# Kernel tuning notes

Hardware: AMD Instinct MI355X
Metric: run time of the kernel (lower is better)

## Reference

```python
import jax, jax.numpy as jnp
import numpy as np

B, T, H, V = 4, 512, 2048, 32000
BETA = 0.1          # KL coefficient vs reference model
EPS_LOW = 0.2       # PPO clip lower
EPS_HIGH = 0.2      # PPO clip upper
TEMP = 1.0          # logit temperature


def _per_token_logps(h, w, ids):
    # h: [B,T,H], w: [V,H], ids: [B,T] -> log p(token_id) per position
    logits = jnp.einsum('bth,vh->btv', h, w) / TEMP          # [B,T,V]
    logps = jax.nn.log_softmax(logits.astype(jnp.float32), axis=-1)
    return jnp.take_along_axis(logps, ids[..., None], axis=-1)[..., 0]  # [B,T]


def setup_inputs() -> dict:
    key = jax.random.key(0)
    k = jax.random.split(key, 6)
    x = jax.random.normal(k[0], (B, T, H), jnp.float32)
    ref_input = jax.random.normal(k[1], (B, T, H), jnp.float32)
    lin_weight = jax.random.normal(k[2], (V, H), jnp.float32) * (H ** -0.5)
    ref_weight = jax.random.normal(k[3], (V, H), jnp.float32) * (H ** -0.5)
    selected_token_ids = jax.random.randint(k[4], (B, T), 0, V)
    attention_mask = jnp.ones((B, T), jnp.int32)
    advantages = jax.random.normal(k[5], (B,), jnp.float32)
    return {
        'x': x,
        'lin_weight': lin_weight,
        'ref_input': ref_input,
        'ref_weight': ref_weight,
        'advantages': advantages,
        'selected_token_ids': selected_token_ids,
        'attention_mask': attention_mask,
    }


def reference(x, lin_weight, ref_input, ref_weight, advantages,
              selected_token_ids, attention_mask):
    # policy per-token log-probs (fused linear + log-softmax + gather)
    logps = _per_token_logps(x, lin_weight, selected_token_ids)            # [B,T]
    # reference model path runs under no_grad in the original
    ref_logps = jax.lax.stop_gradient(
        _per_token_logps(ref_input, ref_weight, selected_token_ids))      # [B,T]
    # old_per_token_logps=None -> detached current logps (ratio==1 in fwd)
    old_logps = jax.lax.stop_gradient(logps)

    coef1 = jnp.exp(logps - old_logps)
    coef2 = jnp.clip(coef1, 1.0 - EPS_LOW, 1.0 + EPS_HIGH)
    adv = advantages[:, None]                                             # [B,1]
    per_token_loss = -jnp.minimum(coef1 * adv, coef2 * adv)

    # KL(ref || policy) surrogate: exp(d) - d - 1 with d = ref - cur
    d = ref_logps - logps
    kl = jnp.exp(d) - d - 1.0
    per_token_loss = per_token_loss + BETA * kl

    mask = attention_mask.astype(jnp.float32)
    # loss_type='bnpo': global masked token mean
    loss = jnp.sum(per_token_loss * mask) / jnp.maximum(jnp.sum(mask), 1.0)
    return loss
```

## Files before the change

### kernel.cpp

```cpp
#include <hip/hip_runtime.h>
#include <hip/hip_bf16.h>

#define B_ 4
#define T_ 512
#define H_ 2048
#define V_ 32000
#define M_ (B_ * T_)
#define BETA_ 0.1f

#define BM 128
#define BN 128
#define BK 32
#define NTILES (V_ / BN)
#define NP (NTILES * 2)
#define NPAD 512
#define GRID_LIN 4096

typedef __attribute__((ext_vector_type(8))) short short8;
typedef __attribute__((ext_vector_type(4))) float f32x4;

__device__ __forceinline__ void async_copy16(const void* g, void* l) {
  __builtin_amdgcn_global_load_lds(
      (const __attribute__((address_space(1))) void*)g,
      (__attribute__((address_space(3))) void*)l, 16, 0, 0);
}

__device__ __forceinline__ unsigned short f2bf(float f) {
  unsigned int u = __float_as_uint(f);
  u += 0x7fffu + ((u >> 16) & 1u);
  return (unsigned short)(u >> 16);
}

__global__ void cvt_bf16_kernel(const float* __restrict__ in,
                                unsigned short* __restrict__ out, int n4) {
  int i = blockIdx.x * blockDim.x + threadIdx.x;
  if (i < n4) {
    float4 v = ((const float4*)in)[i];
    ushort4 o;
    o.x = f2bf(v.x); o.y = f2bf(v.y); o.z = f2bf(v.z); o.w = f2bf(v.w);
    ((ushort4*)out)[i] = o;
  }
}

__global__ void sel_kernel(const float* __restrict__ x, const float* __restrict__ w,
                           const float* __restrict__ rx, const float* __restrict__ rw,
                           const int* __restrict__ ids, float* __restrict__ sel) {
  int gw = (blockIdx.x * 256 + threadIdx.x) >> 6;
  int l = threadIdx.x & 63;
  int md = gw >> 11;
  int m = gw & (M_ - 1);
  const float* xr = (md ? rx : x) + (size_t)m * H_;
  const float* wr = (md ? rw : w) + (size_t)ids[m] * H_;
  float s = 0.0f;
#pragma unroll
  for (int it = 0; it < H_ / 256; ++it) {
    int k = it * 256 + l * 4;
    float4 a = *(const float4*)(xr + k);
    float4 b = *(const float4*)(wr + k);
    s += a.x * b.x + a.y * b.y + a.z * b.z + a.w * b.w;
  }
#pragma unroll
  for (int off = 32; off; off >>= 1) s += __shfl_xor(s, off, 64);
  if (l == 0) sel[md * M_ + m] = s;
}

__global__ __launch_bounds__(256) void gemm_lse_kernel(
    const unsigned short* __restrict__ A,
    const unsigned short* __restrict__ Bw,
    float* __restrict__ pmax,
    float* __restrict__ psum) {
  const int linear = blockIdx.x;
  const int nt = (linear & 7) + 8 * (linear >> 7);
  if (nt >= NTILES) return;
  const int mb = (linear >> 3) & 15;

  __shared__ char smem[(BM + BN) * BK * 2];
  char* As = smem;
  char* Bs = smem + BM * BK * 2;

  const int tid = threadIdx.x;
  const int w = tid >> 6, l = tid & 63;
  const int quad = l >> 4, lr = l & 15;
  const int m0 = mb * BM, n0 = nt * BN;
  const int wm = (w >> 1) * 64, wn = (w & 1) * 64;

  const int s0 = tid, s1 = tid + 256;
  const unsigned short* gA0 = A + (size_t)(m0 + (s0 & 127)) * H_ + (s0 >> 7) * 8;
  const unsigned short* gA1 = A + (size_t)(m0 + (s1 & 127)) * H_ + (s1 >> 7) * 8;
  const unsigned short* gB0 = Bw + (size_t)(n0 + (s0 & 127)) * H_ + (s0 >> 7) * 8;
  const unsigned short* gB1 = Bw + (size_t)(n0 + (s1 & 127)) * H_ + (s1 >> 7) * 8;
  char* lA0 = As + s0 * 16; char* lA1 = As + s1 * 16;
  char* lB0 = Bs + s0 * 16; char* lB1 = Bs + s1 * 16;

  f32x4 acc[4][4] = {};

  const char* aRd[4]; const char* bRd[4];
#pragma unroll
  for (int i = 0; i < 4; ++i) {
    aRd[i] = As + (quad * 128 + wm + i * 16 + lr) * 16;
    bRd[i] = Bs + (quad * 128 + wn + i * 16 + lr) * 16;
  }

  for (int kt = 0; kt < H_ / BK; ++kt) {
    async_copy16(gA0, lA0); async_copy16(gA1, lA1);
    async_copy16(gB0, lB0); async_copy16(gB1, lB1);
    gA0 += BK; gA1 += BK; gB0 += BK; gB1 += BK;
    __syncthreads();
    short8 af[4], bf[4];
#pragma unroll
    for (int i = 0; i < 4; ++i) af[i] = *(const short8*)aRd[i];
#pragma unroll
    for (int j = 0; j < 4; ++j) bf[j] = *(const short8*)bRd[j];
#pragma unroll
    for (int i = 0; i < 4; ++i)
#pragma unroll
      for (int j = 0; j < 4; ++j)
        acc[i][j] = __builtin_amdgcn_mfma_f32_16x16x32_bf16(af[i], bf[j], acc[i][j], 0, 0, 0);
    __syncthreads();
  }

  const int p_idx = nt * 2 + (w & 1);
#pragma unroll
  for (int i = 0; i < 4; ++i) {
#pragma unroll
    for (int r = 0; r < 4; ++r) {
      float vmax = fmaxf(fmaxf(acc[i][0][r], acc[i][1][r]),
                         fmaxf(acc[i][2][r], acc[i][3][r]));
#pragma unroll
      for (int off = 8; off; off >>= 1) vmax = fmaxf(vmax, __shfl_xor(vmax, off, 64));
      float s = __expf(acc[i][0][r] - vmax) + __expf(acc[i][1][r] - vmax) +
                __expf(acc[i][2][r] - vmax) + __expf(acc[i][3][r] - vmax);
#pragma unroll
      for (int off = 8; off; off >>= 1) s += __shfl_xor(s, off, 64);
      if (lr == 0) {
        int mg = m0 + wm + i * 16 + quad * 4 + r;
        pmax[(size_t)mg * NPAD + p_idx] = vmax;
        psum[(size_t)mg * NPAD + p_idx] = s;
      }
    }
  }
}

__global__ void lse_merge_kernel(
    const float* __restrict__ pmaxP, const float* __restrict__ psumP,
    const float* __restrict__ pmaxR, const float* __restrict__ psumR,
    const float* __restrict__ sel, float* __restrict__ lp) {
  int gw = (blockIdx.x * 256 + threadIdx.x) >> 6;
  int l = threadIdx.x & 63;
  int md = gw >> 11, m = gw & (M_ - 1);
  const float* pm = (md ? pmaxR : pmaxP) + (size_t)m * NPAD;
  const float* ps = (md ? psumR : psumP) + (size_t)m * NPAD;
  float mx = -3.0e38f, s = 0.0f;
  for (int p = l; p < NP; p += 64) {
    float a = pm[p], b = ps[p];
    float nm = fmaxf(mx, a);
    s = s * __expf(mx - nm) + b * __expf(a - nm);
    mx = nm;
  }
#pragma unroll
  for (int off = 32; off; off >>= 1) {
    float omx = __shfl_xor(mx, off, 64);
    float os  = __shfl_xor(s, off, 64);
    float nm = fmaxf(mx, omx);
    s = s * __expf(mx - nm) + os * __expf(omx - nm);
    mx = nm;
  }
  if (l == 0) lp[md * M_ + m] = sel[md * M_ + m] - (mx + __logf(s));
}

__global__ void loss_kernel(const float* __restrict__ lp,
                            const float* __restrict__ adv,
                            const int* __restrict__ mask,
                            float* __restrict__ out) {
  __shared__ float sp[16], sm[16];
  int t = threadIdx.x;
  float pt = 0.0f, mk = 0.0f;
  for (int m = t; m < M_; m += 1024) {
    float d = lp[M_ + m] - lp[m];
    float kl = __expf(d) - d - 1.0f;
    float mkm = (float)mask[m];
    pt += (-adv[m >> 9] + BETA_ * kl) * mkm;
    mk += mkm;
  }
#pragma unroll
  for (int off = 32; off; off >>= 1) {
    pt += __shfl_xor(pt, off, 64);
    mk += __shfl_xor(mk, off, 64);
  }
  int wv = t >> 6, l = t & 63;
  if (l == 0) { sp[wv] = pt; sm[wv] = mk; }
  __syncthreads();
  if (t == 0) {
    float a = 0.0f, b = 0.0f;
#pragma unroll
    for (int i = 0; i < 16; ++i) { a += sp[i]; b += sm[i]; }
    out[0] = a / fmaxf(b, 1.0f);
  }
}

extern "C" void kernel_launch(void* const* d_in, const int* in_sizes, int n_in,
                              void* d_out, int out_size, void* d_ws, size_t ws_size,
                              hipStream_t stream) {
  const float* x    = (const float*)d_in[0];
  const float* lw   = (const float*)d_in[1];
  const float* rx   = (const float*)d_in[2];
  const float* rw   = (const float*)d_in[3];
  const float* adv  = (const float*)d_in[4];
  const int*   ids  = (const int*)d_in[5];
  const int*   mask = (const int*)d_in[6];
  float* out = (float*)d_out;

  char* ws = (char*)d_ws;
  unsigned short* Wb = (unsigned short*)ws;
  unsigned short* xb = (unsigned short*)(ws + (size_t)V_ * H_ * 2);
  char* p0 = ws + (size_t)V_ * H_ * 2 + (size_t)M_ * H_ * 2;
  const size_t PSZ = (size_t)M_ * NPAD * 4;
  float* pmaxP = (float*)(p0);
  float* psumP = (float*)(p0 + 1 * PSZ);
  float* pmaxR = (float*)(p0 + 2 * PSZ);
  float* psumR = (float*)(p0 + 3 * PSZ);
  float* sel   = (float*)(p0 + 4 * PSZ);
  float* lp    = (float*)(p0 + 4 * PSZ + 2 * M_ * 4);

  const int n4x = M_ * H_ / 4, n4w = V_ * H_ / 4;

  cvt_bf16_kernel<<<(n4x + 255) / 256, 256, 0, stream>>>(x, xb, n4x);
  cvt_bf16_kernel<<<(n4w + 255) / 256, 256, 0, stream>>>(lw, Wb, n4w);
  sel_kernel<<<(2 * M_) / 4, 256, 0, stream>>>(x, lw, rx, rw, ids, sel);
  gemm_lse_kernel<<<GRID_LIN, 256, 0, stream>>>(xb, Wb, pmaxP, psumP);
  cvt_bf16_kernel<<<(n4x + 255) / 256, 256, 0, stream>>>(rx, xb, n4x);
  cvt_bf16_kernel<<<(n4w + 255) / 256, 256, 0, stream>>>(rw, Wb, n4w);
  gemm_lse_kernel<<<GRID_LIN, 256, 0, stream>>>(xb, Wb, pmaxR, psumR);

  lse_merge_kernel<<<(2 * M_) / 4, 256, 0, stream>>>(pmaxP, psumP, pmaxR, psumR,
                                                     sel, lp);
  loss_kernel<<<1, 1024, 0, stream>>>(lp, adv, mask, out);
}
```

Baseline: 1.665 ms.

## Double-buffer GEMM LDS tiles with async prefetch and merge bf16 conversion launches

After: 1.679 ms. Within noise of the previous version (+0.9%).

```diff
diff --git a/kernel.cpp b/kernel.cpp
--- a/kernel.cpp
+++ b/kernel.cpp
@@ -31,15 +31,18 @@
   return (unsigned short)(u >> 16);
 }
 
-__global__ void cvt_bf16_kernel(const float* __restrict__ in,
-                                unsigned short* __restrict__ out, int n4) {
+__global__ void cvt2_bf16_kernel(const float* __restrict__ inA,
+                                 unsigned short* __restrict__ outA, int n4a,
+                                 const float* __restrict__ inB,
+                                 unsigned short* __restrict__ outB, int n4b) {
   int i = blockIdx.x * blockDim.x + threadIdx.x;
-  if (i < n4) {
-    float4 v = ((const float4*)in)[i];
-    ushort4 o;
-    o.x = f2bf(v.x); o.y = f2bf(v.y); o.z = f2bf(v.z); o.w = f2bf(v.w);
-    ((ushort4*)out)[i] = o;
-  }
+  const float* in; unsigned short* out;
+  if (i < n4a) { in = inA; out = outA; }
+  else { i -= n4a; if (i >= n4b) return; in = inB; out = outB; }
+  float4 v = ((const float4*)in)[i];
+  ushort4 o;
+  o.x = f2bf(v.x); o.y = f2bf(v.y); o.z = f2bf(v.z); o.w = f2bf(v.w);
+  ((ushort4*)out)[i] = o;
 }
 
 __global__ void sel_kernel(const float* __restrict__ x, const float* __restrict__ w,
@@ -74,9 +77,9 @@
   if (nt >= NTILES) return;
   const int mb = (linear >> 3) & 15;
 
-  __shared__ char smem[(BM + BN) * BK * 2];
-  char* As = smem;
-  char* Bs = smem + BM * BK * 2;
+  __shared__ char smem[32768];
+  char* As0 = smem;          char* As1 = smem + 8192;
+  char* Bs0 = smem + 16384;  char* Bs1 = smem + 24576;
 
   const int tid = threadIdx.x;
   const int w = tid >> 6, l = tid & 63;
@@ -85,39 +88,55 @@
   const int wm = (w >> 1) * 64, wn = (w & 1) * 64;
 
   const int s0 = tid, s1 = tid + 256;
+  const int o0 = s0 * 16, o1 = s1 * 16;
   const unsigned short* gA0 = A + (size_t)(m0 + (s0 & 127)) * H_ + (s0 >> 7) * 8;
   const unsigned short* gA1 = A + (size_t)(m0 + (s1 & 127)) * H_ + (s1 >> 7) * 8;
   const unsigned short* gB0 = Bw + (size_t)(n0 + (s0 & 127)) * H_ + (s0 >> 7) * 8;
   const unsigned short* gB1 = Bw + (size_t)(n0 + (s1 & 127)) * H_ + (s1 >> 7) * 8;
-  char* lA0 = As + s0 * 16; char* lA1 = As + s1 * 16;
-  char* lB0 = Bs + s0 * 16; char* lB1 = Bs + s1 * 16;
+
+  async_copy16(gA0, As0 + o0); async_copy16(gA1, As0 + o1);
+  async_copy16(gB0, Bs0 + o0); async_copy16(gB1, Bs0 + o1);
+  gA0 += BK; gA1 += BK; gB0 += BK; gB1 += BK;
+  async_copy16(gA0, As1 + o0); async_copy16(gA1, As1 + o1);
+  async_copy16(gB0, Bs1 + o0); async_copy16(gB1, Bs1 + o1);
+  gA0 += BK; gA1 += BK; gB0 += BK; gB1 += BK;
 
   f32x4 acc[4][4] = {};
 
-  const char* aRd[4]; const char* bRd[4];
+  int aOff[4], bOff[4];
 #pragma unroll
   for (int i = 0; i < 4; ++i) {
-    aRd[i] = As + (quad * 128 + wm + i * 16 + lr) * 16;
-    bRd[i] = Bs + (quad * 128 + wn + i * 16 + lr) * 16;
-  }
-
-  for (int kt = 0; kt < H_ / BK; ++kt) {
-    async_copy16(gA0, lA0); async_copy16(gA1, lA1);
-    async_copy16(gB0, lB0); async_copy16(gB1, lB1);
-    gA0 += BK; gA1 += BK; gB0 += BK; gB1 += BK;
-    __syncthreads();
-    short8 af[4], bf[4];
-#pragma unroll
-    for (int i = 0; i < 4; ++i) af[i] = *(const short8*)aRd[i];
-#pragma unroll
-    for (int j = 0; j < 4; ++j) bf[j] = *(const short8*)bRd[j];
-#pragma unroll
-    for (int i = 0; i < 4; ++i)
-#pragma unroll
-      for (int j = 0; j < 4; ++j)
-        acc[i][j] = __builtin_amdgcn_mfma_f32_16x16x32_bf16(af[i], bf[j], acc[i][j], 0, 0, 0);
-    __syncthreads();
-  }
+    aOff[i] = (quad * 128 + wm + i * 16 + lr) * 16;
+    bOff[i] = (quad * 128 + wn + i * 16 + lr) * 16;
+  }
+
+#define KITER(VMSTR, PRE, AS, BS)                                              \
+  {                                                                            \
+    asm volatile("s_waitcnt vmcnt(" VMSTR ")\n\ts_barrier" ::: "memory");      \
+    short8 af[4], bf[4];                                                       \
+    _Pragma("unroll") for (int i = 0; i < 4; ++i)                              \
+        af[i] = *(const short8*)(AS + aOff[i]);                                \
+    _Pragma("unroll") for (int j = 0; j < 4; ++j)                              \
+        bf[j] = *(const short8*)(BS + bOff[j]);                                \
+    asm volatile("s_waitcnt lgkmcnt(0)\n\ts_barrier" ::: "memory");            \
+    if (PRE) {                                                                 \
+      async_copy16(gA0, AS + o0); async_copy16(gA1, AS + o1);                  \
+      async_copy16(gB0, BS + o0); async_copy16(gB1, BS + o1);                  \
+      gA0 += BK; gA1 += BK; gB0 += BK; gB1 += BK;                              \
+    }                                                                          \
+    _Pragma("unroll") for (int i = 0; i < 4; ++i)                              \
+    _Pragma("unroll") for (int j = 0; j < 4; ++j)                              \
+      acc[i][j] = __builtin_amdgcn_mfma_f32_16x16x32_bf16(af[i], bf[j],        \
+                                                          acc[i][j], 0, 0, 0); \
+  }
+
+  for (int kp = 0; kp < 31; ++kp) {
+    KITER("4", 1, As0, Bs0);
+    KITER("4", 1, As1, Bs1);
+  }
+  KITER("4", 0, As0, Bs0);
+  KITER("0", 0, As1, Bs1);
+#undef KITER
 
   const int p_idx = nt * 2 + (w & 1);
 #pragma unroll
@@ -223,13 +242,12 @@
   float* lp    = (float*)(p0 + 4 * PSZ + 2 * M_ * 4);
 
   const int n4x = M_ * H_ / 4, n4w = V_ * H_ / 4;
-
-  cvt_bf16_kernel<<<(n4x + 255) / 256, 256, 0, stream>>>(x, xb, n4x);
-  cvt_bf16_kernel<<<(n4w + 255) / 256, 256, 0, stream>>>(lw, Wb, n4w);
+  const int cvtg = (n4w + n4x + 255) / 256;
+
+  cvt2_bf16_kernel<<<cvtg, 256, 0, stream>>>(lw, Wb, n4w, x, xb, n4x);
   sel_kernel<<<(2 * M_) / 4, 256, 0, stream>>>(x, lw, rx, rw, ids, sel);
   gemm_lse_kernel<<<GRID_LIN, 256, 0, stream>>>(xb, Wb, pmaxP, psumP);
-  cvt_bf16_kernel<<<(n4x + 255) / 256, 256, 0, stream>>>(rx, xb, n4x);
-  cvt_bf16_kernel<<<(n4w + 255) / 256, 256, 0, stream>>>(rw, Wb, n4w);
+  cvt2_bf16_kernel<<<cvtg, 256, 0, stream>>>(rw, Wb, n4w, rx, xb, n4x);
   gemm_lse_kernel<<<GRID_LIN, 256, 0, stream>>>(xb, Wb, pmaxR, psumR);
 
   lse_merge_kernel<<<(2 * M_) / 4, 256, 0, stream>>>(pmaxP, psumP, pmaxR, psumR,
```
